# Optimization experiments

Measured on AMD Instinct MI355X. Metric: run time of the kernel, lower is better.

The kernel has to match this reference:

```python
import jax, jax.numpy as jnp
import numpy as np

B, D, L = 16384, 2048, 6

def setup_inputs() -> dict:
    key = jax.random.key(0)
    kx, kw = jax.random.split(key)
    x = jax.random.normal(kx, (B, D), dtype=jnp.float32)
    # cross weights: xavier_normal on (D,1) -> std = sqrt(2/(D+1)); stacked [L, D]
    std = float(np.sqrt(2.0 / (D + 1)))
    W = jax.random.normal(kw, (L, D), dtype=jnp.float32) * std
    b = jnp.zeros((L, D), dtype=jnp.float32)  # bias params init to zeros
    return {"x": x, "W": W, "b": b}

def reference(x, W, b):
    # Original per layer: x_l = (x0 @ x_l^T) @ w_i + b_i + x_l
    # Algebraically identical: x_l = x0 * (x_l . w_i) + b_i + x_l  (scalar per row)
    x_l = x
    for i in range(W.shape[0]):
        s = jnp.einsum('bd,d->b', x_l, W[i])          # [B]
        x_l = x * s[:, None] + b[i][None, :] + x_l     # [B, D]
    return x_l
```

## Files before the change

kernel.cpp:

```cpp
#include <hip/hip_runtime.h>

#define B_ROWS   16384
#define D_DIM    2048
#define L_LAYERS 6
#define THREADS  1024
#define WPB      (THREADS / 64)
#define BLOCKS   (B_ROWS / WPB)

typedef float f32x4 __attribute__((ext_vector_type(4)));

__global__ __launch_bounds__(THREADS, 7) void cross_net_kernel(
    const float* __restrict__ x,
    const float* __restrict__ W,
    const float* __restrict__ b,
    float* __restrict__ out)
{
    __shared__ float Wl[L_LAYERS][D_DIM];
    __shared__ float Ul[D_DIM];
    __shared__ float red[WPB][L_LAYERS];
    __shared__ float eL[L_LAYERS];

    const int t    = threadIdx.x;
    const int lane = t & 63;
    const int wid  = t >> 6;

    const int gw   = blockIdx.x * WPB + wid;
    const float* xr = x + (size_t)gw * D_DIM;
    const int eoff = lane * 4;
    float4 xv[8];
    #pragma unroll
    for (int j = 0; j < 8; ++j) xv[j] = *(const float4*)(xr + j * 256 + eoff);

    {
        const int base = t * 2;
        float2 prefix = make_float2(0.f, 0.f);
        float e_red[L_LAYERS];
        #pragma unroll
        for (int l = 0; l < L_LAYERS; ++l) {
            const float2 wv = *(const float2*)(W + l * D_DIM + base);
            const float2 bv = *(const float2*)(b + l * D_DIM + base);
            e_red[l] = prefix.x * wv.x + prefix.y * wv.y;
            prefix.x += bv.x; prefix.y += bv.y;
            *(float2*)&Wl[l][base] = wv;
        }
        *(float2*)&Ul[base] = prefix;
        #pragma unroll
        for (int l = 0; l < L_LAYERS; ++l) {
            float v = e_red[l];
            #pragma unroll
            for (int off = 32; off >= 1; off >>= 1) v += __shfl_xor(v, off, 64);
            if (lane == 0) red[wid][l] = v;
        }
    }
    __syncthreads();
    if (t < L_LAYERS) {
        float s = 0.f;
        #pragma unroll
        for (int w = 0; w < WPB; ++w) s += red[w][t];
        eL[t] = s;
    }
    __syncthreads();

    float p[L_LAYERS];
    #pragma unroll
    for (int l = 0; l < L_LAYERS; ++l) {
        float a = 0.f;
        #pragma unroll
        for (int j = 0; j < 8; ++j) {
            const float4 wv = *(const float4*)&Wl[l][j * 256 + eoff];
            a += xv[j].x * wv.x + xv[j].y * wv.y + xv[j].z * wv.z + xv[j].w * wv.w;
        }
        p[l] = a;
    }

    #pragma unroll
    for (int off = 32; off >= 1; off >>= 1) {
        #pragma unroll
        for (int l = 0; l < L_LAYERS; ++l)
            p[l] += __shfl_xor(p[l], off, 64);
    }

    float c = 1.f;
    #pragma unroll
    for (int l = 0; l < L_LAYERS; ++l)
        c = c * (1.f + p[l]) + eL[l];

    float* orow = out + (size_t)gw * D_DIM;
    #pragma unroll
    for (int j = 0; j < 8; ++j) {
        const float4 uv = *(const float4*)&Ul[j * 256 + eoff];
        f32x4 o;
        o.x = c * xv[j].x + uv.x; o.y = c * xv[j].y + uv.y;
        o.z = c * xv[j].z + uv.z; o.w = c * xv[j].w + uv.w;
        __builtin_nontemporal_store(o, (f32x4*)(orow + j * 256 + eoff));
    }
}

extern "C" void kernel_launch(void* const* d_in, const int* in_sizes, int n_in,
                              void* d_out, int out_size, void* d_ws, size_t ws_size,
                              hipStream_t stream) {
    (void)in_sizes; (void)n_in; (void)d_ws; (void)ws_size; (void)out_size;
    const float* x = (const float*)d_in[0];
    const float* W = (const float*)d_in[1];
    const float* b = (const float*)d_in[2];
    float* out = (float*)d_out;
    cross_net_kernel<<<dim3(BLOCKS), dim3(THREADS), 0, stream>>>(x, W, b, out);
}
```

Before: 300.0 us.

## Split bias precompute into separate kernel and shrink row blocks to 256 threads

A single-block precompute kernel writes the bias prefix sums and correction terms into the workspace. The row kernel then drops from 1024 to 256 threads per block and reads W straight from global memory (through the cache) instead of staging it in LDS. This cuts per-block setup work and LDS use, which should allow more resident blocks. In exchange it adds a second launch and repeated global or L2 reads of W. If no workspace is available, a fallback path recomputes the values in every block.

```diff
diff --git a/kernel.cpp b/kernel.cpp
--- a/kernel.cpp
+++ b/kernel.cpp
@@ -3,47 +3,93 @@
 #define B_ROWS   16384
 #define D_DIM    2048
 #define L_LAYERS 6
-#define THREADS  1024
-#define WPB      (THREADS / 64)
-#define BLOCKS   (B_ROWS / WPB)
+
+#define ROW_THREADS 256
+#define ROW_WAVES   (ROW_THREADS / 64)
+#define ROW_BLOCKS  (B_ROWS / ROW_WAVES)
+#define PRE_THREADS 1024
+#define WS_FLOATS   (D_DIM + L_LAYERS)
 
 typedef float f32x4 __attribute__((ext_vector_type(4)));
 
-__global__ __launch_bounds__(THREADS, 7) void cross_net_kernel(
+
+__global__ __launch_bounds__(PRE_THREADS) void precompute_Ue(
+    const float* __restrict__ W,
+    const float* __restrict__ b,
+    float* __restrict__ ws)
+{
+    __shared__ float red[PRE_THREADS / 64][L_LAYERS];
+    const int t    = threadIdx.x;
+    const int lane = t & 63;
+    const int wid  = t >> 6;
+    const int base = t * 2;
+
+    float2 prefix = make_float2(0.f, 0.f);
+    float e_red[L_LAYERS];
+    #pragma unroll
+    for (int l = 0; l < L_LAYERS; ++l) {
+        const float2 wv = *(const float2*)(W + l * D_DIM + base);
+        const float2 bv = *(const float2*)(b + l * D_DIM + base);
+        e_red[l] = prefix.x * wv.x + prefix.y * wv.y;
+        prefix.x += bv.x; prefix.y += bv.y;
+    }
+    *(float2*)(ws + base) = prefix;
+    #pragma unroll
+    for (int l = 0; l < L_LAYERS; ++l) {
+        float v = e_red[l];
+        #pragma unroll
+        for (int off = 32; off >= 1; off >>= 1) v += __shfl_xor(v, off, 64);
+        if (lane == 0) red[wid][l] = v;
+    }
+    __syncthreads();
+    if (t < L_LAYERS) {
+        float s = 0.f;
+        #pragma unroll
+        for (int w = 0; w < PRE_THREADS / 64; ++w) s += red[w][t];
+        ws[D_DIM + t] = s;
+    }
+}
+
+template <bool USE_WS>
+__global__ __launch_bounds__(ROW_THREADS) void cross_rows(
     const float* __restrict__ x,
     const float* __restrict__ W,
     const float* __restrict__ b,
+    const float* __restrict__ ws,
     float* __restrict__ out)
 {
-    __shared__ float Wl[L_LAYERS][D_DIM];
     __shared__ float Ul[D_DIM];
-    __shared__ float red[WPB][L_LAYERS];
-    __shared__ float eL[L_LAYERS];
+    __shared__ float eLs[L_LAYERS];
+    __shared__ float red[ROW_WAVES][L_LAYERS];
 
     const int t    = threadIdx.x;
     const int lane = t & 63;
     const int wid  = t >> 6;
 
-    const int gw   = blockIdx.x * WPB + wid;
-    const float* xr = x + (size_t)gw * D_DIM;
-    const int eoff = lane * 4;
-    float4 xv[8];
-    #pragma unroll
-    for (int j = 0; j < 8; ++j) xv[j] = *(const float4*)(xr + j * 256 + eoff);
-
-    {
-        const int base = t * 2;
-        float2 prefix = make_float2(0.f, 0.f);
+    if constexpr (USE_WS) {
+        const int base = t * 8;
+        *(float4*)&Ul[base]     = *(const float4*)(ws + base);
+        *(float4*)&Ul[base + 4] = *(const float4*)(ws + base + 4);
+        if (t < L_LAYERS) eLs[t] = ws[D_DIM + t];
+        __syncthreads();
+    } else {
+        const int base = t * 8;
+        float4 p0 = make_float4(0.f, 0.f, 0.f, 0.f);
+        float4 p1 = make_float4(0.f, 0.f, 0.f, 0.f);
         float e_red[L_LAYERS];
         #pragma unroll
         for (int l = 0; l < L_LAYERS; ++l) {
-            const float2 wv = *(const float2*)(W + l * D_DIM + base);
-            const float2 bv = *(const float2*)(b + l * D_DIM + base);
-            e_red[l] = prefix.x * wv.x + prefix.y * wv.y;
-            prefix.x += bv.x; prefix.y += bv.y;
-            *(float2*)&Wl[l][base] = wv;
+            const float4 w0 = *(const float4*)(W + l * D_DIM + base);
+            const float4 w1 = *(const float4*)(W + l * D_DIM + base + 4);
+            const float4 b0 = *(const float4*)(b + l * D_DIM + base);
+            const float4 b1 = *(const float4*)(b + l * D_DIM + base + 4);
+            e_red[l] = p0.x * w0.x + p0.y * w0.y + p0.z * w0.z + p0.w * w0.w
+                     + p1.x * w1.x + p1.y * w1.y + p1.z * w1.z + p1.w * w1.w;
+            p0.x += b0.x; p0.y += b0.y; p0.z += b0.z; p0.w += b0.w;
+            p1.x += b1.x; p1.y += b1.y; p1.z += b1.z; p1.w += b1.w;
         }
-        *(float2*)&Ul[base] = prefix;
+        *(float4*)&Ul[base]     = p0;
+        *(float4*)&Ul[base + 4] = p1;
         #pragma unroll
         for (int l = 0; l < L_LAYERS; ++l) {
             float v = e_red[l];
@@ -51,15 +97,23 @@
             for (int off = 32; off >= 1; off >>= 1) v += __shfl_xor(v, off, 64);
             if (lane == 0) red[wid][l] = v;
         }
+        __syncthreads();
+        if (t < L_LAYERS) {
+            float s = 0.f;
+            #pragma unroll
+            for (int w = 0; w < ROW_WAVES; ++w) s += red[w][t];
+            eLs[t] = s;
+        }
+        __syncthreads();
     }
-    __syncthreads();
-    if (t < L_LAYERS) {
-        float s = 0.f;
-        #pragma unroll
-        for (int w = 0; w < WPB; ++w) s += red[w][t];
-        eL[t] = s;
-    }
-    __syncthreads();
+
+    const int gw   = blockIdx.x * ROW_WAVES + wid;
+    const float* xr = x + (size_t)gw * D_DIM;
+    const int eoff = lane * 4;
+
+    float4 xv[8];
+    #pragma unroll
+    for (int j = 0; j < 8; ++j) xv[j] = *(const float4*)(xr + j * 256 + eoff);
 
     float p[L_LAYERS];
     #pragma unroll
@@ -67,7 +121,7 @@
         float a = 0.f;
         #pragma unroll
         for (int j = 0; j < 8; ++j) {
-            const float4 wv = *(const float4*)&Wl[l][j * 256 + eoff];
+            const float4 wv = *(const float4*)(W + l * D_DIM + j * 256 + eoff);
             a += xv[j].x * wv.x + xv[j].y * wv.y + xv[j].z * wv.z + xv[j].w * wv.w;
         }
         p[l] = a;
@@ -83,7 +137,7 @@
     float c = 1.f;
     #pragma unroll
     for (int l = 0; l < L_LAYERS; ++l)
-        c = c * (1.f + p[l]) + eL[l];
+        c = c * (1.f + p[l]) + eLs[l];
 
     float* orow = out + (size_t)gw * D_DIM;
     #pragma unroll
@@ -99,10 +153,20 @@
 extern "C" void kernel_launch(void* const* d_in, const int* in_sizes, int n_in,
                               void* d_out, int out_size, void* d_ws, size_t ws_size,
                               hipStream_t stream) {
-    (void)in_sizes; (void)n_in; (void)d_ws; (void)ws_size; (void)out_size;
+    (void)in_sizes; (void)n_in; (void)out_size;
     const float* x = (const float*)d_in[0];
     const float* W = (const float*)d_in[1];
     const float* b = (const float*)d_in[2];
     float* out = (float*)d_out;
-    cross_net_kernel<<<dim3(BLOCKS), dim3(THREADS), 0, stream>>>(x, W, b, out);
+
+    const bool use_ws = (d_ws != nullptr) && (ws_size >= WS_FLOATS * sizeof(float));
+    if (use_ws) {
+        float* ws = (float*)d_ws;
+        precompute_Ue<<<dim3(1), dim3(PRE_THREADS), 0, stream>>>(W, b, ws);
+        cross_rows<true><<<dim3(ROW_BLOCKS), dim3(ROW_THREADS), 0, stream>>>(
+            x, W, b, ws, out);
+    } else {
+        cross_rows<false><<<dim3(ROW_BLOCKS), dim3(ROW_THREADS), 0, stream>>>(
+            x, W, b, nullptr, out);
+    }
 }
```

New measurement: 251.7 us. -16.1%, faster.
